# Kernel optimization log

Hardware: AMD Instinct MI355X
Metric: run time of the kernel (lower is better)

Reference implementation:

```python
import jax, jax.numpy as jnp
import numpy as np

B, N_PER, D = 128, 512, 128        # graphs, nodes per graph, feature width
N = B * N_PER                      # 65536 total nodes
E = 524288                         # total edges (avg degree 8)
KS = (410, 328, 263)               # ceil(0.8*512), ceil(0.8*410), ceil(0.8*328)


def setup_inputs() -> dict:
    key = jax.random.key(0)
    ks = jax.random.split(key, 20)
    p = lambda k, shape: jax.random.normal(k, shape, jnp.float32) * 0.05
    rng = np.random.default_rng(0)
    g = rng.integers(0, B, size=E)
    s = rng.integers(0, N_PER, size=E)
    t = rng.integers(0, N_PER, size=E)
    edge_index = jnp.asarray(np.stack([g * N_PER + s, g * N_PER + t]).astype(np.int32))
    inp = {
        'x': jax.random.normal(ks[0], (N, 1, D), jnp.float32),
        'edge_index': edge_index,
    }
    i = 1
    for l in (1, 2, 3):
        inp[f'conv{l}_wl'] = p(ks[i], (D, D)); i += 1   # SAGEConv lin_l (neighbors) weight
        inp[f'conv{l}_bl'] = p(ks[i], (D,));  i += 1   # SAGEConv lin_l bias
        inp[f'conv{l}_wr'] = p(ks[i], (D, D)); i += 1   # SAGEConv lin_r (root) weight
        inp[f'pool{l}_w'] = p(ks[i], (D,));   i += 1   # TopKPooling score vector
    inp['lin1_w'] = p(ks[13], (128, 256)); inp['lin1_b'] = p(ks[14], (128,))
    inp['lin2_w'] = p(ks[15], (64, 128));  inp['lin2_b'] = p(ks[16], (64,))
    inp['lin3_w'] = p(ks[17], (1, 64));    inp['lin3_b'] = p(ks[18], (1,))
    return inp


def _sage(x, node_mask, src, dst, wl, bl, wr):
    # SAGEConv, mean aggregation: lin_l(mean_{j->i} x_j) + lin_r(x_i)
    em = (node_mask[src] & node_mask[dst]).astype(x.dtype)   # [E] valid-edge mask
    msum = jax.ops.segment_sum(x[src] * em[:, None], dst, num_segments=N)
    deg = jax.ops.segment_sum(em, dst, num_segments=N)
    mean = msum / jnp.maximum(deg, 1.0)[:, None]
    return mean @ wl.T + bl + x @ wr.T


def _topk_pool(x, node_mask, w, k):
    # TopKPooling: score = x.w/||w||; keep top-k per graph; gate kept x by tanh(score)
    score = (x @ w) / (jnp.linalg.norm(w) + 1e-16)           # [N]
    score = jnp.where(node_mask, score, -jnp.inf)
    _, idx = jax.lax.top_k(score.reshape(B, N_PER), k)       # [B, k] within-graph ids
    nm = jnp.zeros((B, N_PER), bool).at[jnp.arange(B)[:, None], idx].set(True).reshape(-1)
    x = jnp.where(nm[:, None], x * jnp.tanh(score)[:, None], 0.0)
    return x, nm


def _readout(x, node_mask, k):
    # cat([global_max_pool, global_mean_pool]) over the k surviving nodes per graph
    xb = x.reshape(B, N_PER, -1)
    mb = node_mask.reshape(B, N_PER, 1)
    gmax = jnp.max(jnp.where(mb, xb, -jnp.inf), axis=1)
    gmean = jnp.sum(jnp.where(mb, xb, 0.0), axis=1) / k
    return jnp.concatenate([gmax, gmean], axis=1)            # [B, 2D]


def _forward(edge_index, x, conv1_wl, conv1_bl, conv1_wr, pool1_w,
             conv2_wl, conv2_bl, conv2_wr, pool2_w,
             conv3_wl, conv3_bl, conv3_wr, pool3_w,
             lin1_w, lin1_b, lin2_w, lin2_b, lin3_w, lin3_b):
    src, dst = edge_index[0], edge_index[1]
    h = x[:, 0, :]                                           # x.squeeze(1) -> [N, D]
    nm = jnp.ones((N,), bool)
    layers = ((conv1_wl, conv1_bl, conv1_wr, pool1_w),
              (conv2_wl, conv2_bl, conv2_wr, pool2_w),
              (conv3_wl, conv3_bl, conv3_wr, pool3_w))
    reads = []
    for (wl, bl, wr, pw), k in zip(layers, KS):
        h = jax.nn.relu(_sage(h, nm, src, dst, wl, bl, wr))
        h, nm = _topk_pool(h, nm, pw, k)
        reads.append(_readout(h, nm, float(k)))
    z = reads[0] + reads[1] + reads[2]                       # [B, 256]
    z = jax.nn.relu(z @ lin1_w.T + lin1_b)
    z = jax.nn.relu(z @ lin2_w.T + lin2_b)
    # dropout p=0.5 is a no-op at eval time
    return jax.nn.sigmoid(z @ lin3_w.T + lin3_b)[:, 0]       # [B]


def reference(x, edge_index, conv1_wl, conv1_bl, conv1_wr, pool1_w,
              conv2_wl, conv2_bl, conv2_wr, pool2_w,
              conv3_wl, conv3_bl, conv3_wr, pool3_w,
              lin1_w, lin1_b, lin2_w, lin2_b, lin3_w, lin3_b):
    return _forward(edge_index, x, conv1_wl, conv1_bl, conv1_wr, pool1_w,
                    conv2_wl, conv2_bl, conv2_wr, pool2_w,
                    conv3_wl, conv3_bl, conv3_wr, pool3_w,
                    lin1_w, lin1_b, lin2_w, lin2_b, lin3_w, lin3_b)
```

## Files before the change

kernel.cpp:

```cpp
#include <hip/hip_runtime.h>
#include <math.h>

#define NND 65536
#define NPER 512
#define NGR 128
#define DD 128
#define NED 524288

typedef __attribute__((ext_vector_type(8))) short short8;
typedef __attribute__((ext_vector_type(4))) float f32x4;

__device__ __forceinline__ unsigned short f2b(float f) {
  unsigned u = __float_as_uint(f);
  return (unsigned short)((u + 0x7FFFu + ((u >> 16) & 1u)) >> 16);
}
__device__ __forceinline__ float b2f(unsigned short h) {
  return __uint_as_float(((unsigned)h) << 16);
}


__global__ __launch_bounds__(256) void init_kernel(int* __restrict__ counts,
                                                   int* __restrict__ mask) {
  int i = blockIdx.x * 256 + threadIdx.x;
  counts[i] = 0;
  mask[i] = 1;
}

__global__ __launch_bounds__(256) void hist_kernel(const int* __restrict__ ei,
                                                   int* __restrict__ counts) {
  int e = blockIdx.x * 256 + threadIdx.x;
  atomicAdd(&counts[ei[NED + e]], 1);
}

__global__ __launch_bounds__(1024) void scan_kernel(const int* __restrict__ counts,
                                                    int* __restrict__ off,
                                                    int* __restrict__ cursor) {
  __shared__ int part[1024];
  int t = threadIdx.x;
  int base = t * 64;
  int s = 0;
  for (int i = 0; i < 64; ++i) s += counts[base + i];
  part[t] = s;
  __syncthreads();
  for (int d = 1; d < 1024; d <<= 1) {
    int v = (t >= d) ? part[t - d] : 0;
    __syncthreads();
    part[t] += v;
    __syncthreads();
  }
  int run = (t == 0) ? 0 : part[t - 1];
  for (int i = 0; i < 64; ++i) {
    off[base + i] = run;
    cursor[base + i] = run;
    run += counts[base + i];
  }
  if (t == 1023) off[NND] = run;
}

__global__ __launch_bounds__(256) void scatter_kernel(const int* __restrict__ ei,
                                                      int* __restrict__ cursor,
                                                      int* __restrict__ ssrc) {
  int e = blockIdx.x * 256 + threadIdx.x;
  int dst = ei[NED + e];
  int pos = atomicAdd(&cursor[dst], 1);
  ssrc[pos] = ei[e];
}


__global__ __launch_bounds__(256) void prepw_kernel(
    const float* __restrict__ wl0, const float* __restrict__ wr0,
    const float* __restrict__ wl1, const float* __restrict__ wr1,
    const float* __restrict__ wl2, const float* __restrict__ wr2,
    unsigned short* __restrict__ Whi, unsigned short* __restrict__ Wlo) {
  const float* wls[3] = {wl0, wl1, wl2};
  const float* wrs[3] = {wr0, wr1, wr2};
  int e = blockIdx.x * 256 + threadIdx.x;
  int l = e >> 15;
  int o = e & 32767;
  int j = o & 7;
  int lane = (o >> 3) & 63;
  int nt = (o >> 9) & 7;
  int kc = o >> 12;
  int li = lane & 15, q = lane >> 4;
  int n = nt * 16 + li;
  int k = kc * 32 + q * 8 + j;
  const float* src = (k < 128) ? wls[l] : wrs[l];
  float v = src[n * DD + (k & 127)];
  unsigned short hi = f2b(v);
  float lo = v - b2f(hi);
  Whi[e] = hi;
  Wlo[e] = f2b(lo);
}


template <int CM>
__global__ __launch_bounds__(256) void agg_kernel_t(const float* __restrict__ x,
                                                    const int* __restrict__ mask,
                                                    const int* __restrict__ off,
                                                    const int* __restrict__ ssrc,
                                                    float* __restrict__ mean) {
  const int wave = threadIdx.x >> 6;
  const int lane = threadIdx.x & 63;
  const int half = lane >> 5;
  const int l = lane & 31;
  const int bid = blockIdx.x;
  const int xcd = bid & 7;
  const int slot = bid >> 3;
  const int graph = xcd * 16 + (slot >> 7);
  const int within = slot & 127;
  const int dst = graph * NPER + within * 4 + wave;

  if (CM && !mask[dst]) {
    if (lane < 32) *(float4*)(mean + (size_t)dst * DD + l * 4) = make_float4(0.f, 0.f, 0.f, 0.f);
    return;
  }
  const int beg = off[dst], end = off[dst + 1];
  float4 acc = make_float4(0.f, 0.f, 0.f, 0.f);
  int deg = 0;
  for (int base = beg; base < end; base += 64) {
    const int n = min(64, end - base);
    int sv = 0, mv = 0;
    if (lane < n) {
      sv = ssrc[base + lane];
      if (CM) mv = mask[sv];
    }
    if (CM)
      deg += (int)__popcll(__ballot(mv != 0));
    else
      deg += n;
    for (int j = half; j < n; j += 2) {
      const int s = __shfl(sv, j);
      const float4 v = *(const float4*)(x + (size_t)s * DD + l * 4);
      acc.x += v.x;
      acc.y += v.y;
      acc.z += v.z;
      acc.w += v.w;
    }
  }
  acc.x += __shfl(acc.x, lane ^ 32);
  acc.y += __shfl(acc.y, lane ^ 32);
  acc.z += __shfl(acc.z, lane ^ 32);
  acc.w += __shfl(acc.w, lane ^ 32);
  const float inv = 1.f / (float)max(deg, 1);
  if (lane < 32) {
    float4 m;
    m.x = acc.x * inv;
    m.y = acc.y * inv;
    m.z = acc.z * inv;
    m.w = acc.w * inv;
    *(float4*)(mean + (size_t)dst * DD + l * 4) = m;
  }
}


#define GBM 64

__global__ __launch_bounds__(256) void gemm_kernel(
    const float* __restrict__ Amean, const float* __restrict__ Ax,
    const unsigned short* __restrict__ Whi, const unsigned short* __restrict__ Wlo,
    const float* __restrict__ bias, const float* __restrict__ pw,
    float* __restrict__ outp, float* __restrict__ sraw) {
  __shared__ short Ah[2048];
  __shared__ short Al[2048];
  __shared__ float s_sp[4][GBM];
  const int tid = threadIdx.x;
  const int wv = tid >> 6;
  const int lane = tid & 63;
  const int q = lane >> 4;
  const int li = lane & 15;
  const int row0 = blockIdx.x * GBM;

  int sdst[2];
#pragma unroll
  for (int i = 0; i < 2; ++i) {
    const int id = tid + i * 256;
    const int r = id >> 3;
    const int kb = (id & 7) << 2;
    sdst[i] = ((r >> 4) * 64 + (kb >> 3) * 16 + (r & 15)) * 8 + (kb & 7);
  }

  f32x4 acc[4][2];
#pragma unroll
  for (int m = 0; m < 4; ++m)
#pragma unroll
    for (int n = 0; n < 2; ++n) acc[m][n] = (f32x4){0.f, 0.f, 0.f, 0.f};

  float4 pa[2];
  short8 pbh[2], pbl[2];

#define LOADA(KC)                                                                    \
  {                                                                                  \
    const float* Asrc = ((KC) < 4) ? Amean : Ax;                                     \
    const int cb = ((KC) & 3) * 32;                                                  \
    _Pragma("unroll") for (int i = 0; i < 2; ++i) {                                  \
      const int id = tid + i * 256;                                                  \
      pa[i] = *(const float4*)(Asrc + (size_t)(row0 + (id >> 3)) * DD + cb + ((id & 7) << 2)); \
    }                                                                                \
  }
#define LOADB(KC)                                                                    \
  {                                                                                  \
    _Pragma("unroll") for (int n = 0; n < 2; ++n) {                                  \
      const int ga = (((KC)*8 + wv * 2 + n) * 64 + lane) * 8;                        \
      pbh[n] = *(const short8*)(Whi + ga);                                           \
      pbl[n] = *(const short8*)(Wlo + ga);                                           \
    }                                                                                \
  }

  LOADA(0) LOADB(0)

#pragma unroll
  for (int kc = 0; kc < 8; ++kc) {
#pragma unroll
    for (int i = 0; i < 2; ++i) {
      ushort4 hv, lv;
      hv.x = f2b(pa[i].x); lv.x = f2b(pa[i].x - b2f(hv.x));
      hv.y = f2b(pa[i].y); lv.y = f2b(pa[i].y - b2f(hv.y));
      hv.z = f2b(pa[i].z); lv.z = f2b(pa[i].z - b2f(hv.z));
      hv.w = f2b(pa[i].w); lv.w = f2b(pa[i].w - b2f(hv.w));
      *(ushort4*)(Ah + sdst[i]) = hv;
      *(ushort4*)(Al + sdst[i]) = lv;
    }
    short8 bh[2], bl[2];
    bh[0] = pbh[0]; bh[1] = pbh[1];
    bl[0] = pbl[0]; bl[1] = pbl[1];
    __syncthreads();
    short8 ah[4], al[4];
#pragma unroll
    for (int m = 0; m < 4; ++m) {
      ah[m] = *(const short8*)(Ah + (m * 64 + lane) * 8);
      al[m] = *(const short8*)(Al + (m * 64 + lane) * 8);
    }
    if (kc < 7) { LOADA(kc + 1) LOADB(kc + 1) }
#pragma unroll
    for (int m = 0; m < 4; ++m)
#pragma unroll
      for (int n = 0; n < 2; ++n) {
        acc[m][n] = __builtin_amdgcn_mfma_f32_16x16x32_bf16(ah[m], bh[n], acc[m][n], 0, 0, 0);
        acc[m][n] = __builtin_amdgcn_mfma_f32_16x16x32_bf16(ah[m], bl[n], acc[m][n], 0, 0, 0);
        acc[m][n] = __builtin_amdgcn_mfma_f32_16x16x32_bf16(al[m], bh[n], acc[m][n], 0, 0, 0);
      }
    __syncthreads();
  }
#undef LOADA
#undef LOADB

  const int c0 = wv * 32 + li;
  const int c1 = wv * 32 + 16 + li;
  const float b0 = bias[c0], b1 = bias[c1];
  const float p0 = pw[c0], p1 = pw[c1];
  float sp[16];
#pragma unroll
  for (int m = 0; m < 4; ++m) {
#pragma unroll
    for (int i = 0; i < 4; ++i) {
      const int r = row0 + m * 16 + q * 4 + i;
      const float v0 = fmaxf(acc[m][0][i] + b0, 0.f);
      const float v1 = fmaxf(acc[m][1][i] + b1, 0.f);
      outp[(size_t)r * DD + c0] = v0;
      outp[(size_t)r * DD + c1] = v1;
      sp[m * 4 + i] = v0 * p0 + v1 * p1;
    }
  }
#pragma unroll
  for (int e = 0; e < 16; ++e) {
    sp[e] += __shfl_xor(sp[e], 1);
    sp[e] += __shfl_xor(sp[e], 2);
    sp[e] += __shfl_xor(sp[e], 4);
    sp[e] += __shfl_xor(sp[e], 8);
  }
  if (li == 0) {
#pragma unroll
    for (int e = 0; e < 16; ++e) s_sp[wv][(e >> 2) * 16 + q * 4 + (e & 3)] = sp[e];
  }
  __syncthreads();
  if (tid < GBM)
    sraw[row0 + tid] = s_sp[0][tid] + s_sp[1][tid] + s_sp[2][tid] + s_sp[3][tid];
}


__global__ __launch_bounds__(256) void pool_kernel(float* __restrict__ h,
                                                   const float* __restrict__ sraw,
                                                   const float* __restrict__ pw,
                                                   const int* __restrict__ maskP,
                                                   int* __restrict__ maskN,
                                                   float* __restrict__ zp,
                                                   const int kk) {
  __shared__ float s_sc[NPER];
  __shared__ float s_t[128];
  __shared__ unsigned char s_sel[128];
  __shared__ float red[4 * 128];
  __shared__ float s_norm;
  const int b = blockIdx.x;
  const int g = b >> 2;
  const int q = b & 3;
  const int tid = threadIdx.x;
  const int lane = tid & 63;

  if (tid < 64) {
    const float v0 = pw[lane], v1 = pw[lane + 64];
    float p = v0 * v0 + v1 * v1;
#pragma unroll
    for (int o = 32; o > 0; o >>= 1) p += __shfl_down(p, o);
    if (lane == 0) s_norm = 1.f / (sqrtf(p) + 1e-16f);
  }
  __syncthreads();
  const float inv_norm = s_norm;
#pragma unroll
  for (int i = 0; i < 2; ++i) {
    const int n = tid + i * 256;
    const int node = g * NPER + n;
    s_sc[n] = maskP[node] ? sraw[node] * inv_norm : -INFINITY;
  }
  __syncthreads();

  if (tid < 128) {
    const int n = q * 128 + tid;
    const float s = s_sc[n];
    int rank = 0;
    for (int j = 0; j < NPER; ++j) {
      const float sj = s_sc[j];
      rank += (sj > s || (sj == s && j < n)) ? 1 : 0;
    }
    const int sel = (rank < kk) ? 1 : 0;
    maskN[g * NPER + n] = sel;
    s_sel[tid] = (unsigned char)sel;
    s_t[tid] = sel ? tanhf(s) : 0.f;
  }
  __syncthreads();

  const int fcol = tid & 127;
  const int off = tid >> 7;
  float pmax = -INFINITY;
  float psum = 0.f;
  const int nbase = g * NPER + q * 128;
  for (int i = 0; i < 64; ++i) {
    const int nl = off + 2 * i;
    float* hp = h + (size_t)(nbase + nl) * DD + fcol;
    const float t = s_t[nl];
    const float v = *hp * t;
    *hp = v;
    psum += v;
    if (s_sel[nl]) pmax = fmaxf(pmax, v);
  }
  red[off * 128 + fcol] = pmax;
  red[256 + off * 128 + fcol] = psum;
  __syncthreads();
  if (tid < 128) {
    float* row = zp + (size_t)b * 256;
    row[tid] = fmaxf(red[tid], red[128 + tid]);
    row[128 + tid] = red[256 + tid] + red[384 + tid];
  }
}


__global__ __launch_bounds__(128) void mlp_kernel(const float* __restrict__ zpart,
                                                  const float* __restrict__ w1,
                                                  const float* __restrict__ b1,
                                                  const float* __restrict__ w2,
                                                  const float* __restrict__ b2,
                                                  const float* __restrict__ w3,
                                                  const float* __restrict__ b3,
                                                  float* __restrict__ out,
                                                  const float ik0, const float ik1,
                                                  const float ik2) {
  __shared__ float z[256];
  __shared__ float h1[128];
  __shared__ float h2[64];
  const int g = blockIdx.x;
  const int t = threadIdx.x;
  const float iks[3] = {ik0, ik1, ik2};
  float zmax = 0.f, zmean = 0.f;
#pragma unroll
  for (int l = 0; l < 3; ++l) {
    const float* zp = zpart + ((size_t)l * 512 + g * 4) * 256;
    zmax += fmaxf(fmaxf(zp[t], zp[256 + t]), fmaxf(zp[512 + t], zp[768 + t]));
    zmean += (zp[128 + t] + zp[384 + t] + zp[640 + t] + zp[896 + t]) * iks[l];
  }
  z[t] = zmax;
  z[128 + t] = zmean;
  __syncthreads();
  float a = b1[t];
  for (int k = 0; k < 256; ++k) a = fmaf(z[k], w1[t * 256 + k], a);
  h1[t] = fmaxf(a, 0.f);
  __syncthreads();
  if (t < 64) {
    float a2 = b2[t];
    for (int k = 0; k < 128; ++k) a2 = fmaf(h1[k], w2[t * 128 + k], a2);
    h2[t] = fmaxf(a2, 0.f);
  }
  __syncthreads();
  if (t == 0) {
    float a3 = b3[0];
    for (int k = 0; k < 64; ++k) a3 = fmaf(h2[k], w3[k], a3);
    out[g] = 1.f / (1.f + expf(-a3));
  }
}


extern "C" void kernel_launch(void* const* d_in, const int* in_sizes, int n_in,
                              void* d_out, int out_size, void* d_ws, size_t ws_size,
                              hipStream_t stream) {
  (void)in_sizes; (void)n_in; (void)out_size; (void)ws_size;
  const float* x_in = (const float*)d_in[0];
  const int* ei = (const int*)d_in[1];
  const float* wl[3] = {(const float*)d_in[2], (const float*)d_in[6], (const float*)d_in[10]};
  const float* cbl[3] = {(const float*)d_in[3], (const float*)d_in[7], (const float*)d_in[11]};
  const float* wr[3] = {(const float*)d_in[4], (const float*)d_in[8], (const float*)d_in[12]};
  const float* pw[3] = {(const float*)d_in[5], (const float*)d_in[9], (const float*)d_in[13]};
  const float* l1w = (const float*)d_in[14];
  const float* l1b = (const float*)d_in[15];
  const float* l2w = (const float*)d_in[16];
  const float* l2b = (const float*)d_in[17];
  const float* l3w = (const float*)d_in[18];
  const float* l3b = (const float*)d_in[19];
  float* out = (float*)d_out;

  char* w = (char*)d_ws;
  int* counts = (int*)(w + 0 * (1 << 20));
  int* off = (int*)(w + 1 * (1 << 20));
  int* cursor = (int*)(w + 2 * (1 << 20));
  float* sraw = (float*)(w + 2 * (1 << 20));
  int* maskA = (int*)(w + 3 * (1 << 20));
  int* maskB = (int*)(w + 3 * (1 << 20) + (1 << 19));
  float* zpart = (float*)(w + 4 * (1 << 20));
  unsigned short* Whi = (unsigned short*)(w + 5 * (1 << 20) + (1 << 19));
  unsigned short* Wlo = (unsigned short*)(w + 5 * (1 << 20) + 3 * (1 << 18));
  int* ssrc = (int*)(w + 6 * (1 << 20));
  float* mean = (float*)(w + (size_t)8 * (1 << 20));
  float* hA = (float*)(w + (size_t)40 * (1 << 20));
  float* hB = (float*)(w + (size_t)72 * (1 << 20));

  init_kernel<<<NND / 256, 256, 0, stream>>>(counts, maskA);
  hist_kernel<<<NED / 256, 256, 0, stream>>>(ei, counts);
  scan_kernel<<<1, 1024, 0, stream>>>(counts, off, cursor);
  scatter_kernel<<<NED / 256, 256, 0, stream>>>(ei, cursor, ssrc);
  prepw_kernel<<<384, 256, 0, stream>>>(wl[0], wr[0], wl[1], wr[1], wl[2], wr[2], Whi, Wlo);

  const int ks[3] = {410, 328, 263};
  const float* xl = x_in;
  float* houts[3] = {hA, hB, hA};
  int* mprev[3] = {maskA, maskB, maskA};
  int* mnext[3] = {maskB, maskA, maskB};
  for (int l = 0; l < 3; ++l) {
    float* hout = houts[l];
    if (l == 0)
      agg_kernel_t<0><<<NND / 4, 256, 0, stream>>>(xl, mprev[l], off, ssrc, mean);
    else
      agg_kernel_t<1><<<NND / 4, 256, 0, stream>>>(xl, mprev[l], off, ssrc, mean);
    gemm_kernel<<<NND / GBM, 256, 0, stream>>>(mean, xl, Whi + (size_t)l * 32768,
                                               Wlo + (size_t)l * 32768, cbl[l], pw[l],
                                               hout, sraw);
    pool_kernel<<<NGR * 4, 256, 0, stream>>>(hout, sraw, pw[l], mprev[l], mnext[l],
                                             zpart + (size_t)l * 512 * 256, ks[l]);
    xl = hout;
  }
  mlp_kernel<<<NGR, 128, 0, stream>>>(zpart, l1w, l1b, l2w, l2b, l3w, l3b, out,
                                      1.f / 410.f, 1.f / 328.f, 1.f / 263.f);
}
```

Before: 427.2 us.

## Defer tanh gating into consumers and stop rewriting h in pool kernel

The pool kernel no longer scales and writes h back in place. It now stores a (mask, tanh score) pair per node, and the next layer's aggregation and GEMM apply that gate on the fly when they read h. This removes a full read-modify-write pass over the activations in each pool step. The change also splits the top-k rank loop across 256 threads, vectorises the pooling readout with float4 loads that skip unselected rows, unrolls the neighbor gather by four, and vectorises the count sum in the scan. In exchange, the agg and GEMM loaders do extra multiplies and read an 8-byte gate per node instead of a 4-byte mask.

```diff
diff --git a/kernel.cpp b/kernel.cpp
--- a/kernel.cpp
+++ b/kernel.cpp
@@ -20,10 +20,10 @@
 
 
 __global__ __launch_bounds__(256) void init_kernel(int* __restrict__ counts,
-                                                   int* __restrict__ mask) {
+                                                   float2* __restrict__ tm) {
   int i = blockIdx.x * 256 + threadIdx.x;
   counts[i] = 0;
-  mask[i] = 1;
+  tm[i] = make_float2(1.f, 1.f);
 }
 
 __global__ __launch_bounds__(256) void hist_kernel(const int* __restrict__ ei,
@@ -39,7 +39,11 @@
   int t = threadIdx.x;
   int base = t * 64;
   int s = 0;
-  for (int i = 0; i < 64; ++i) s += counts[base + i];
+  const int4* c4 = (const int4*)(counts + base);
+  for (int i = 0; i < 16; ++i) {
+    int4 v = c4[i];
+    s += v.x + v.y + v.z + v.w;
+  }
   part[t] = s;
   __syncthreads();
   for (int d = 1; d < 1024; d <<= 1) {
@@ -95,7 +99,7 @@
 
 template <int CM>
 __global__ __launch_bounds__(256) void agg_kernel_t(const float* __restrict__ x,
-                                                    const int* __restrict__ mask,
+                                                    const float2* __restrict__ tm,
                                                     const int* __restrict__ off,
                                                     const int* __restrict__ ssrc,
                                                     float* __restrict__ mean) {
@@ -110,7 +114,7 @@
   const int within = slot & 127;
   const int dst = graph * NPER + within * 4 + wave;
 
-  if (CM && !mask[dst]) {
+  if (CM && tm[dst].x == 0.f) {
     if (lane < 32) *(float4*)(mean + (size_t)dst * DD + l * 4) = make_float4(0.f, 0.f, 0.f, 0.f);
     return;
   }
@@ -119,22 +123,60 @@
   int deg = 0;
   for (int base = beg; base < end; base += 64) {
     const int n = min(64, end - base);
-    int sv = 0, mv = 0;
+    int sv = 0;
+    float tv = 0.f;
+    int live = 0;
     if (lane < n) {
       sv = ssrc[base + lane];
-      if (CM) mv = mask[sv];
+      if (CM) {
+        const float2 mt = tm[sv];
+        live = (mt.x != 0.f);
+        tv = mt.y;
+      }
     }
     if (CM)
-      deg += (int)__popcll(__ballot(mv != 0));
+      deg += (int)__popcll(__ballot(live));
     else
       deg += n;
-    for (int j = half; j < n; j += 2) {
+    int j = half;
+    for (; j + 6 < n; j += 8) {
+      const int s0 = __shfl(sv, j);
+      const int s1 = __shfl(sv, j + 2);
+      const int s2 = __shfl(sv, j + 4);
+      const int s3 = __shfl(sv, j + 6);
+      const float4 v0 = *(const float4*)(x + (size_t)s0 * DD + l * 4);
+      const float4 v1 = *(const float4*)(x + (size_t)s1 * DD + l * 4);
+      const float4 v2 = *(const float4*)(x + (size_t)s2 * DD + l * 4);
+      const float4 v3 = *(const float4*)(x + (size_t)s3 * DD + l * 4);
+      if (CM) {
+        const float t0 = __shfl(tv, j), t1 = __shfl(tv, j + 2);
+        const float t2 = __shfl(tv, j + 4), t3 = __shfl(tv, j + 6);
+        acc.x += v0.x * t0 + v1.x * t1 + v2.x * t2 + v3.x * t3;
+        acc.y += v0.y * t0 + v1.y * t1 + v2.y * t2 + v3.y * t3;
+        acc.z += v0.z * t0 + v1.z * t1 + v2.z * t2 + v3.z * t3;
+        acc.w += v0.w * t0 + v1.w * t1 + v2.w * t2 + v3.w * t3;
+      } else {
+        acc.x += v0.x + v1.x + v2.x + v3.x;
+        acc.y += v0.y + v1.y + v2.y + v3.y;
+        acc.z += v0.z + v1.z + v2.z + v3.z;
+        acc.w += v0.w + v1.w + v2.w + v3.w;
+      }
+    }
+    for (; j < n; j += 2) {
       const int s = __shfl(sv, j);
       const float4 v = *(const float4*)(x + (size_t)s * DD + l * 4);
-      acc.x += v.x;
-      acc.y += v.y;
-      acc.z += v.z;
-      acc.w += v.w;
+      if (CM) {
+        const float t = __shfl(tv, j);
+        acc.x += v.x * t;
+        acc.y += v.y * t;
+        acc.z += v.z * t;
+        acc.w += v.w * t;
+      } else {
+        acc.x += v.x;
+        acc.y += v.y;
+        acc.z += v.z;
+        acc.w += v.w;
+      }
     }
   }
   acc.x += __shfl(acc.x, lane ^ 32);
@@ -155,8 +197,10 @@
 
 #define GBM 64
 
-__global__ __launch_bounds__(256) void gemm_kernel(
+template <int SCALE>
+__global__ __launch_bounds__(256) void gemm_kernel_t(
     const float* __restrict__ Amean, const float* __restrict__ Ax,
+    const float2* __restrict__ tmp,
     const unsigned short* __restrict__ Whi, const unsigned short* __restrict__ Wlo,
     const float* __restrict__ bias, const float* __restrict__ pw,
     float* __restrict__ outp, float* __restrict__ sraw) {
@@ -195,6 +239,10 @@
     _Pragma("unroll") for (int i = 0; i < 2; ++i) {                                  \
       const int id = tid + i * 256;                                                  \
       pa[i] = *(const float4*)(Asrc + (size_t)(row0 + (id >> 3)) * DD + cb + ((id & 7) << 2)); \
+      if (SCALE && (KC) >= 4) {                                                      \
+        const float tt = tmp[row0 + (id >> 3)].y;                                    \
+        pa[i].x *= tt; pa[i].y *= tt; pa[i].z *= tt; pa[i].w *= tt;                   \
+      }                                                                              \
     }                                                                                \
   }
 #define LOADB(KC)                                                                    \
@@ -278,17 +326,18 @@
 }
 
 
-__global__ __launch_bounds__(256) void pool_kernel(float* __restrict__ h,
+__global__ __launch_bounds__(256) void pool_kernel(const float* __restrict__ h,
                                                    const float* __restrict__ sraw,
                                                    const float* __restrict__ pw,
-                                                   const int* __restrict__ maskP,
-                                                   int* __restrict__ maskN,
+                                                   const float2* __restrict__ tmP,
+                                                   float2* __restrict__ tmN,
                                                    float* __restrict__ zp,
                                                    const int kk) {
   __shared__ float s_sc[NPER];
   __shared__ float s_t[128];
   __shared__ unsigned char s_sel[128];
-  __shared__ float red[4 * 128];
+  __shared__ int s_rk[256];
+  __shared__ float4 red4[512];
   __shared__ float s_norm;
   const int b = blockIdx.x;
   const int g = b >> 2;
@@ -309,46 +358,69 @@
   for (int i = 0; i < 2; ++i) {
     const int n = tid + i * 256;
     const int node = g * NPER + n;
-    s_sc[n] = maskP[node] ? sraw[node] * inv_norm : -INFINITY;
-  }
-  __syncthreads();
-
+    s_sc[n] = (tmP[node].x != 0.f) ? sraw[node] * inv_norm : -INFINITY;
+  }
+  __syncthreads();
+
+  {
+    const int n = q * 128 + (tid & 127);
+    const int jb = (tid >> 7) * 256;
+    const float s = s_sc[n];
+    int rank = 0;
+    for (int j = jb; j < jb + 256; ++j) {
+      const float sj = s_sc[j];
+      rank += (sj > s || (sj == s && j < n)) ? 1 : 0;
+    }
+    s_rk[tid] = rank;
+  }
+  __syncthreads();
   if (tid < 128) {
     const int n = q * 128 + tid;
+    const int rank = s_rk[tid] + s_rk[tid + 128];
+    const int sel = (rank < kk) ? 1 : 0;
     const float s = s_sc[n];
-    int rank = 0;
-    for (int j = 0; j < NPER; ++j) {
-      const float sj = s_sc[j];
-      rank += (sj > s || (sj == s && j < n)) ? 1 : 0;
-    }
-    const int sel = (rank < kk) ? 1 : 0;
-    maskN[g * NPER + n] = sel;
+    const float t = sel ? tanhf(s) : 0.f;
+    tmN[g * NPER + n] = make_float2(sel ? 1.f : 0.f, t);
     s_sel[tid] = (unsigned char)sel;
-    s_t[tid] = sel ? tanhf(s) : 0.f;
-  }
-  __syncthreads();
-
-  const int fcol = tid & 127;
-  const int off = tid >> 7;
-  float pmax = -INFINITY;
-  float psum = 0.f;
-  const int nbase = g * NPER + q * 128;
-  for (int i = 0; i < 64; ++i) {
-    const int nl = off + 2 * i;
-    float* hp = h + (size_t)(nbase + nl) * DD + fcol;
-    const float t = s_t[nl];
-    const float v = *hp * t;
-    *hp = v;
-    psum += v;
-    if (s_sel[nl]) pmax = fmaxf(pmax, v);
-  }
-  red[off * 128 + fcol] = pmax;
-  red[256 + off * 128 + fcol] = psum;
-  __syncthreads();
-  if (tid < 128) {
-    float* row = zp + (size_t)b * 256;
-    row[tid] = fmaxf(red[tid], red[128 + tid]);
-    row[128 + tid] = red[256 + tid] + red[384 + tid];
+    s_t[tid] = t;
+  }
+  __syncthreads();
+
+  const int c = tid & 31;
+  const int r = tid >> 5;
+  float4 pmax = make_float4(-INFINITY, -INFINITY, -INFINITY, -INFINITY);
+  float4 psum = make_float4(0.f, 0.f, 0.f, 0.f);
+  const size_t nbase = (size_t)g * NPER + q * 128;
+  const float4* h4 = (const float4*)h;
+  for (int i = 0; i < 16; ++i) {
+    const int nl = r + 8 * i;
+    if (s_sel[nl]) {
+      float4 v = h4[(nbase + nl) * 32 + c];
+      const float t = s_t[nl];
+      v.x *= t; v.y *= t; v.z *= t; v.w *= t;
+      pmax.x = fmaxf(pmax.x, v.x);
+      pmax.y = fmaxf(pmax.y, v.y);
+      pmax.z = fmaxf(pmax.z, v.z);
+      pmax.w = fmaxf(pmax.w, v.w);
+      psum.x += v.x; psum.y += v.y; psum.z += v.z; psum.w += v.w;
+    }
+  }
+  red4[r * 32 + c] = pmax;
+  red4[256 + r * 32 + c] = psum;
+  __syncthreads();
+  if (tid < 32) {
+    float4 m = red4[tid];
+    float4 sm = red4[256 + tid];
+#pragma unroll
+    for (int rr = 1; rr < 8; ++rr) {
+      const float4 a = red4[rr * 32 + tid];
+      const float4 s2 = red4[256 + rr * 32 + tid];
+      m.x = fmaxf(m.x, a.x); m.y = fmaxf(m.y, a.y);
+      m.z = fmaxf(m.z, a.z); m.w = fmaxf(m.w, a.w);
+      sm.x += s2.x; sm.y += s2.y; sm.z += s2.z; sm.w += s2.w;
+    }
+    *(float4*)(zp + (size_t)b * 256 + tid * 4) = m;
+    *(float4*)(zp + (size_t)b * 256 + 128 + tid * 4) = sm;
   }
 }
 
@@ -420,8 +492,8 @@
   int* off = (int*)(w + 1 * (1 << 20));
   int* cursor = (int*)(w + 2 * (1 << 20));
   float* sraw = (float*)(w + 2 * (1 << 20));
-  int* maskA = (int*)(w + 3 * (1 << 20));
-  int* maskB = (int*)(w + 3 * (1 << 20) + (1 << 19));
+  float2* tmA = (float2*)(w + 3 * (1 << 20));
+  float2* tmB = (float2*)(w + 3 * (1 << 20) + (1 << 19));
   float* zpart = (float*)(w + 4 * (1 << 20));
   unsigned short* Whi = (unsigned short*)(w + 5 * (1 << 20) + (1 << 19));
   unsigned short* Wlo = (unsigned short*)(w + 5 * (1 << 20) + 3 * (1 << 18));
@@ -430,7 +502,7 @@
   float* hA = (float*)(w + (size_t)40 * (1 << 20));
   float* hB = (float*)(w + (size_t)72 * (1 << 20));
 
-  init_kernel<<<NND / 256, 256, 0, stream>>>(counts, maskA);
+  init_kernel<<<NND / 256, 256, 0, stream>>>(counts, tmA);
   hist_kernel<<<NED / 256, 256, 0, stream>>>(ei, counts);
   scan_kernel<<<1, 1024, 0, stream>>>(counts, off, cursor);
   scatter_kernel<<<NED / 256, 256, 0, stream>>>(ei, cursor, ssrc);
@@ -439,18 +511,24 @@
   const int ks[3] = {410, 328, 263};
   const float* xl = x_in;
   float* houts[3] = {hA, hB, hA};
-  int* mprev[3] = {maskA, maskB, maskA};
-  int* mnext[3] = {maskB, maskA, maskB};
+  float2* tprev[3] = {tmA, tmB, tmA};
+  float2* tnext[3] = {tmB, tmA, tmB};
   for (int l = 0; l < 3; ++l) {
     float* hout = houts[l];
-    if (l == 0)
-      agg_kernel_t<0><<<NND / 4, 256, 0, stream>>>(xl, mprev[l], off, ssrc, mean);
-    else
-      agg_kernel_t<1><<<NND / 4, 256, 0, stream>>>(xl, mprev[l], off, ssrc, mean);
-    gemm_kernel<<<NND / GBM, 256, 0, stream>>>(mean, xl, Whi + (size_t)l * 32768,
-                                               Wlo + (size_t)l * 32768, cbl[l], pw[l],
-                                               hout, sraw);
-    pool_kernel<<<NGR * 4, 256, 0, stream>>>(hout, sraw, pw[l], mprev[l], mnext[l],
+    if (l == 0) {
+      agg_kernel_t<0><<<NND / 4, 256, 0, stream>>>(xl, tprev[l], off, ssrc, mean);
+      gemm_kernel_t<0><<<NND / GBM, 256, 0, stream>>>(mean, xl, tprev[l],
+                                                      Whi + (size_t)l * 32768,
+                                                      Wlo + (size_t)l * 32768, cbl[l], pw[l],
+                                                      hout, sraw);
+    } else {
+      agg_kernel_t<1><<<NND / 4, 256, 0, stream>>>(xl, tprev[l], off, ssrc, mean);
+      gemm_kernel_t<1><<<NND / GBM, 256, 0, stream>>>(mean, xl, tprev[l],
+                                                      Whi + (size_t)l * 32768,
+                                                      Wlo + (size_t)l * 32768, cbl[l], pw[l],
+                                                      hout, sraw);
+    }
+    pool_kernel<<<NGR * 4, 256, 0, stream>>>(hout, sraw, pw[l], tprev[l], tnext[l],
                                              zpart + (size_t)l * 512 * 256, ks[l]);
     xl = hout;
   }
```

Result: no change. 420.0 us (-1.7%).
